# Optimization experiments

Hardware: AMD Instinct MI355X
Metric: run time of the kernel (lower is better)

The kernel has to match this reference:

```python
import jax, jax.numpy as jnp
import numpy as np

HIDDEN = 2048
NUM_HEADS = 16
KEY_DIM = 1024      # hidden * expand_k (0.5)
VALUE_DIM = 2048    # hidden * expand_v (1.0)
HEAD_K = KEY_DIM // NUM_HEADS   # 64
HEAD_V = VALUE_DIM // NUM_HEADS # 128
EPS = 1e-5
B, T = 8, 4096


def _rmsnorm(x, w, eps=EPS):
    var = jnp.mean(jnp.square(x), axis=-1, keepdims=True)
    return x * jax.lax.rsqrt(var + eps) * w


def setup_inputs() -> dict:
    key = jax.random.key(0)
    ks = jax.random.split(key, 7)
    s = 1.0 / np.sqrt(HIDDEN)
    return {
        "hidden_states": jax.random.normal(ks[0], (B, T, HIDDEN), dtype=jnp.float32),
        "recurrent_state": jax.random.normal(ks[1], (B, NUM_HEADS, HEAD_K, HEAD_V), dtype=jnp.float32),
        "norm_w": jnp.ones((HIDDEN,), dtype=jnp.float32),
        "q_w": jax.random.uniform(ks[2], (KEY_DIM, HIDDEN), jnp.float32, -s, s),
        "v_norm_w": jnp.ones((HEAD_V,), dtype=jnp.float32),
        "o_w": jax.random.uniform(ks[3], (HIDDEN, VALUE_DIM), jnp.float32, -s, s),
        "gate_w": jax.random.uniform(ks[4], (HIDDEN, HIDDEN), jnp.float32, -s, s),
    }


def reference(hidden_states, recurrent_state, norm_w, q_w, v_norm_w, o_w, gate_w):
    x = _rmsnorm(hidden_states, norm_w)                       # (B,T,D)
    q = x @ q_w.T                                             # (B,T,KEY_DIM)
    q = q.reshape(*q.shape[:2], NUM_HEADS, HEAD_K)            # (B,T,H,K)
    # L2 normalize along last dim (F.normalize default eps=1e-12 on the norm)
    norm = jnp.maximum(jnp.linalg.norm(q, axis=-1, keepdims=True), 1e-12)
    q = q / norm
    o = jnp.einsum('bthk,bhkv->bthv', q, recurrent_state)     # (B,T,H,V)
    o = _rmsnorm(o, v_norm_w)
    o = o.reshape(*o.shape[:2], VALUE_DIM)                    # (B,T,VALUE_DIM)
    o = o @ o_w.T                                             # (B,T,D)
    gate = jax.nn.sigmoid(x @ gate_w.T)                       # (B,T,D)
    return gate * o
```

## Files before the change

kernel.cpp:

```cpp
#include <hip/hip_runtime.h>

typedef unsigned short u16;
typedef unsigned int u32;
typedef __attribute__((ext_vector_type(4))) float f32x4;
typedef __attribute__((ext_vector_type(8))) short short8;
typedef __attribute__((ext_vector_type(4))) short short4v;

#define HIDDEN 2048
#define NHEADS 16
#define KEYDIM 1024
#define VALDIM 2048
#define HEADK 64
#define HEADV 128
#define NBATCH 8
#define SEQ 4096
#define NTOK (NBATCH * SEQ)

__device__ __forceinline__ u16 f2bf(float f) {
  union { float f; u32 u; } c; c.f = f;
  u32 r = c.u + 0x7FFFu + ((c.u >> 16) & 1u);
  return (u16)(r >> 16);
}
__device__ __forceinline__ float bf2f(u16 h) {
  union { u32 u; float f; } c; c.u = ((u32)h) << 16;
  return c.f;
}

__global__ __launch_bounds__(256) void cast_bf16_k(const float* __restrict__ in,
                                                   u16* __restrict__ out, int n4) {
  int i = blockIdx.x * blockDim.x + threadIdx.x;
  if (i >= n4) return;
  f32x4 v = *(const f32x4*)(in + (size_t)i * 4);
  short4v o;
  o[0] = (short)f2bf(v[0]); o[1] = (short)f2bf(v[1]);
  o[2] = (short)f2bf(v[2]); o[3] = (short)f2bf(v[3]);
  *(short4v*)(out + (size_t)i * 4) = o;
}

__global__ __launch_bounds__(256) void rmsnorm_cast_k(const float* __restrict__ x,
                                                      const float* __restrict__ w,
                                                      u16* __restrict__ xb) {
  int r = blockIdx.x;
  int tid = threadIdx.x;
  const float* xp = x + (size_t)r * HIDDEN + tid * 8;
  f32x4 v0 = *(const f32x4*)xp;
  f32x4 v1 = *(const f32x4*)(xp + 4);
  float ss = v0[0]*v0[0]+v0[1]*v0[1]+v0[2]*v0[2]+v0[3]*v0[3]
           + v1[0]*v1[0]+v1[1]*v1[1]+v1[2]*v1[2]+v1[3]*v1[3];
  #pragma unroll
  for (int m = 32; m >= 1; m >>= 1) ss += __shfl_xor(ss, m);
  __shared__ float red[4];
  if ((tid & 63) == 0) red[tid >> 6] = ss;
  __syncthreads();
  float tot = red[0] + red[1] + red[2] + red[3];
  float inv = rsqrtf(tot * (1.0f / HIDDEN) + 1e-5f);
  const float* wp = w + tid * 8;
  f32x4 w0 = *(const f32x4*)wp;
  f32x4 w1 = *(const f32x4*)(wp + 4);
  short8 o;
  o[0] = (short)f2bf(v0[0] * inv * w0[0]);
  o[1] = (short)f2bf(v0[1] * inv * w0[1]);
  o[2] = (short)f2bf(v0[2] * inv * w0[2]);
  o[3] = (short)f2bf(v0[3] * inv * w0[3]);
  o[4] = (short)f2bf(v1[0] * inv * w1[0]);
  o[5] = (short)f2bf(v1[1] * inv * w1[1]);
  o[6] = (short)f2bf(v1[2] * inv * w1[2]);
  o[7] = (short)f2bf(v1[3] * inv * w1[3]);
  *(short8*)(xb + (size_t)r * HIDDEN + tid * 8) = o;
}


__device__ __forceinline__ void gload16(const u16* g, u16* l) {
  __builtin_amdgcn_global_load_lds((const __attribute__((address_space(1))) void*)g,
                                   (__attribute__((address_space(3))) void*)l, 16, 0, 0);
}

#define BAR()                                  \
  do {                                         \
    asm volatile("" ::: "memory");             \
    __builtin_amdgcn_s_barrier();              \
    asm volatile("" ::: "memory");             \
  } while (0)

template <int MODE>
__global__ __launch_bounds__(512, 2) void gemm1b_k(const u16* __restrict__ A,
                                                   const u16* __restrict__ Bw,
                                                   void* __restrict__ Cptr,
                                                   const u16* __restrict__ Gate,
                                                   int M, int N, int K) {
  extern __shared__ u16 lds[];
  const int tid = threadIdx.x;
  const int wid = tid >> 6;
  const int wm = wid >> 2;
  const int wn = wid & 3;
  const int l = tid & 63;
  const int lr = l & 15;
  const int kq = l >> 4;

  const int ntn = N >> 8;
  const int per = gridDim.x >> 3;
  const int b = blockIdx.x;
  const int sidx = (b & 7) * per + (b >> 3);
  const int mt = sidx / ntn;
  const int nt = sidx - mt * ntn;

  const u16* Ag = A + (size_t)(mt * 256) * K;
  const u16* Bg = Bw + (size_t)(nt * 256) * K;

  const int srow = tid >> 3;
  const int schunk = (tid & 7) ^ (srow & 7);

#define STAGE_A(c, h)                                                          \
  do {                                                                         \
    const u16* _s = Ag + (size_t)((h) * 128 + srow) * K + ((c) << 6) + schunk * 8; \
    u16* _d = lds + (((c) & 1) << 15) + (h) * 8192 + tid * 8;                  \
    gload16(_s, _d);                                                           \
    gload16(_s + (size_t)64 * K, _d + 4096);                                   \
  } while (0)
#define STAGE_B(c, h)                                                          \
  do {                                                                         \
    const u16* _s = Bg + (size_t)((h) * 128 + srow) * K + ((c) << 6) + schunk * 8; \
    u16* _d = lds + (((c) & 1) << 15) + 16384 + (h) * 8192 + tid * 8;          \
    gload16(_s, _d);                                                           \
    gload16(_s + (size_t)64 * K, _d + 4096);                                   \
  } while (0)

  const int c0s = (kq ^ (lr & 7)) << 3;
  const int c1s = ((4 + kq) ^ (lr & 7)) << 3;
  const int aRowBase = (wm * 128 + lr) * 64;
  const int bRowBase = (wn * 64 + lr) * 64;

  short8 afr[4][2];
  short8 bfr[2][2][2];
  f32x4 acc[8][4] = {};

  auto LDA = [&](int buf, int mh) {
    #pragma unroll
    for (int mi = 0; mi < 4; ++mi) {
      const u16* p = lds + (buf << 15) + aRowBase + (mh * 64 + mi * 16) * 64;
      afr[mi][0] = *(const short8*)(p + c0s);
      afr[mi][1] = *(const short8*)(p + c1s);
    }
  };
  auto LDB_ALL = [&](int buf) {
    #pragma unroll
    for (int nh = 0; nh < 2; ++nh) {
      #pragma unroll
      for (int ni = 0; ni < 2; ++ni) {
        const u16* p = lds + (buf << 15) + 16384 + bRowBase + ((nh * 2 + ni) * 16) * 64;
        bfr[nh][ni][0] = *(const short8*)(p + c0s);
        bfr[nh][ni][1] = *(const short8*)(p + c1s);
      }
    }
  };
  auto MMA = [&](int mh, int nh) {
    __builtin_amdgcn_s_setprio(1);
    #pragma unroll
    for (int mi = 0; mi < 4; ++mi) {
      #pragma unroll
      for (int ni = 0; ni < 2; ++ni) {
        int m = mh * 4 + mi, n = nh * 2 + ni;
        acc[m][n] = __builtin_amdgcn_mfma_f32_16x16x32_bf16(afr[mi][0], bfr[nh][ni][0], acc[m][n], 0, 0, 0);
        acc[m][n] = __builtin_amdgcn_mfma_f32_16x16x32_bf16(afr[mi][1], bfr[nh][ni][1], acc[m][n], 0, 0, 0);
      }
    }
    __builtin_amdgcn_s_setprio(0);
  };

  STAGE_A(0, 0); STAGE_A(0, 1);
  STAGE_B(0, 0); STAGE_B(0, 1);
  STAGE_B(1, 0); STAGE_B(1, 1);
  asm volatile("s_waitcnt vmcnt(4)" ::: "memory");
  BAR();

  const int NITER = K >> 7;
  for (int i = 0; i < NITER; ++i) {
    const int g = (i + 1 < NITER);
    const int cA = 2 * i + 1, c2 = 2 * i + 2, c3 = 2 * i + 3;

    LDB_ALL(0); LDA(0, 0);
    STAGE_A(cA, 0);
    BAR(); MMA(0, 0);
    STAGE_A(cA, 1);
    BAR(); MMA(0, 1);
    LDA(0, 1);
    if (g) STAGE_B(c2, 0);
    BAR(); MMA(1, 1);
    if (g) {
      STAGE_B(c2, 1);
      asm volatile("s_waitcnt vmcnt(4)" ::: "memory");
    } else {
      asm volatile("s_waitcnt vmcnt(0)" ::: "memory");
    }
    BAR(); MMA(1, 0);

    LDB_ALL(1); LDA(1, 0);
    if (g) STAGE_A(c2, 0);
    BAR(); MMA(0, 0);
    if (g) STAGE_A(c2, 1);
    BAR(); MMA(0, 1);
    LDA(1, 1);
    if (g) STAGE_B(c3, 0);
    BAR(); MMA(1, 1);
    if (g) {
      STAGE_B(c3, 1);
      asm volatile("s_waitcnt vmcnt(4)" ::: "memory");
    }
    BAR(); MMA(1, 0);
  }
#undef STAGE_A
#undef STAGE_B

  const int rowB = mt * 256 + wm * 128 + kq * 4;
  const int colB = nt * 256 + wn * 64 + lr;
  #pragma unroll
  for (int m = 0; m < 8; ++m) {
    #pragma unroll
    for (int n = 0; n < 4; ++n) {
      #pragma unroll
      for (int j = 0; j < 4; ++j) {
        int row = rowB + m * 16 + j;
        int col = colB + n * 16;
        size_t idx = (size_t)row * N + col;
        float v = acc[m][n][j];
        if constexpr (MODE == 0) {
          ((u16*)Cptr)[idx] = f2bf(v);
        } else if constexpr (MODE == 1) {
          ((u16*)Cptr)[idx] = f2bf(1.0f / (1.0f + __expf(-v)));
        } else if constexpr (MODE == 2) {
          ((float*)Cptr)[idx] = v * bf2f(Gate[idx]);
        } else if constexpr (MODE == 3) {
          ((float*)Cptr)[idx] = 1.0f / (1.0f + __expf(-v));
        } else {
          float* O = (float*)Cptr;
          O[idx] = O[idx] * v;
        }
      }
    }
  }
}

__global__ __launch_bounds__(256) void glaread_k(const u16* __restrict__ q,
                                                 const float* __restrict__ S,
                                                 const float* __restrict__ vw,
                                                 u16* __restrict__ omid) {
  int bh = blockIdx.x;
  int b = bh >> 4, h = bh & 15;
  int tid = threadIdx.x;
  int w = tid >> 6, l = tid & 63;
  int lr = l & 15, kq = l >> 4;

  const float* Sp = S + (size_t)bh * HEADK * HEADV;
  short8 bfrag[8][2];
  #pragma unroll
  for (int n = 0; n < 8; ++n) {
    #pragma unroll
    for (int s = 0; s < 2; ++s) {
      #pragma unroll
      for (int i = 0; i < 8; ++i)
        bfrag[n][s][i] =
            (short)f2bf(Sp[(size_t)(s * 32 + kq * 8 + i) * HEADV + n * 16 + lr]);
    }
  }
  float vwn[8];
  #pragma unroll
  for (int n = 0; n < 8; ++n) vwn[n] = vw[n * 16 + lr];

  #pragma unroll 1
  for (int it = 0; it < 8; ++it) {
    int t0 = blockIdx.y * 512 + it * 64 + w * 16;
    const u16* qp = q + (size_t)(b * SEQ + t0 + lr) * KEYDIM + h * HEADK;
    short8 a0 = *(const short8*)(qp + kq * 8);
    short8 a1 = *(const short8*)(qp + 32 + kq * 8);

    float ss = 0.f;
    #pragma unroll
    for (int i = 0; i < 8; ++i) {
      float x0 = bf2f((u16)a0[i]), x1 = bf2f((u16)a1[i]);
      ss += x0 * x0 + x1 * x1;
    }
    ss += __shfl_xor(ss, 16);
    ss += __shfl_xor(ss, 32);
    float sc = 1.0f / fmaxf(sqrtf(ss), 1e-12f);

    short8 an0, an1;
    #pragma unroll
    for (int i = 0; i < 8; ++i) {
      an0[i] = (short)f2bf(bf2f((u16)a0[i]) * sc);
      an1[i] = (short)f2bf(bf2f((u16)a1[i]) * sc);
    }

    f32x4 acc[8] = {};
    #pragma unroll
    for (int n = 0; n < 8; ++n) {
      acc[n] = __builtin_amdgcn_mfma_f32_16x16x32_bf16(an0, bfrag[n][0], acc[n], 0, 0, 0);
      acc[n] = __builtin_amdgcn_mfma_f32_16x16x32_bf16(an1, bfrag[n][1], acc[n], 0, 0, 0);
    }

    float part[4] = {0.f, 0.f, 0.f, 0.f};
    #pragma unroll
    for (int n = 0; n < 8; ++n) {
      #pragma unroll
      for (int j = 0; j < 4; ++j) part[j] += acc[n][j] * acc[n][j];
    }
    #pragma unroll
    for (int msk = 1; msk <= 8; msk <<= 1) {
      #pragma unroll
      for (int j = 0; j < 4; ++j) part[j] += __shfl_xor(part[j], msk);
    }
    #pragma unroll
    for (int j = 0; j < 4; ++j) {
      float inv = rsqrtf(part[j] * (1.0f / HEADV) + 1e-5f);
      int tok = t0 + kq * 4 + j;
      u16* op = omid + (size_t)(b * SEQ + tok) * VALDIM + h * HEADV;
      #pragma unroll
      for (int n = 0; n < 8; ++n)
        op[n * 16 + lr] = f2bf(acc[n][j] * inv * vwn[n]);
    }
  }
}

extern "C" void kernel_launch(void* const* d_in, const int* in_sizes, int n_in,
                              void* d_out, int out_size, void* d_ws, size_t ws_size,
                              hipStream_t stream) {
  const float* hs = (const float*)d_in[0];
  const float* S  = (const float*)d_in[1];
  const float* nw = (const float*)d_in[2];
  const float* qw = (const float*)d_in[3];
  const float* vw = (const float*)d_in[4];
  const float* ow = (const float*)d_in[5];
  const float* gw = (const float*)d_in[6];
  float* out = (float*)d_out;

  u16* xb   = (u16*)d_ws;
  u16* q    = xb + (size_t)NTOK * HIDDEN;
  u16* qwb  = q + (size_t)NTOK * KEYDIM;
  u16* owb  = qwb + (size_t)KEYDIM * HIDDEN;
  u16* gwb  = owb + (size_t)HIDDEN * VALDIM;
  u16* gatebuf = gwb + (size_t)HIDDEN * HIDDEN;
  u16* omid = xb;

  const size_t need = ((size_t)NTOK * HIDDEN * 2) * 2 + (size_t)NTOK * KEYDIM * 2 +
                      ((size_t)KEYDIM * HIDDEN + 2 * (size_t)HIDDEN * HIDDEN) * 2;
  const bool bigws = ws_size >= need;

  const size_t LDSB = 131072;

  cast_bf16_k<<<(KEYDIM * HIDDEN / 4 + 255) / 256, 256, 0, stream>>>(qw, qwb, KEYDIM * HIDDEN / 4);
  cast_bf16_k<<<(HIDDEN * VALDIM / 4 + 255) / 256, 256, 0, stream>>>(ow, owb, HIDDEN * VALDIM / 4);
  cast_bf16_k<<<(HIDDEN * HIDDEN / 4 + 255) / 256, 256, 0, stream>>>(gw, gwb, HIDDEN * HIDDEN / 4);

  rmsnorm_cast_k<<<NTOK, 256, 0, stream>>>(hs, nw, xb);

  gemm1b_k<0><<<dim3((NTOK / 256) * (KEYDIM / 256)), 512, LDSB, stream>>>(xb, qwb, q, nullptr, NTOK, KEYDIM, HIDDEN);

  if (bigws) {
    gemm1b_k<1><<<dim3((NTOK / 256) * (HIDDEN / 256)), 512, LDSB, stream>>>(xb, gwb, gatebuf, nullptr, NTOK, HIDDEN, HIDDEN);
  } else {
    gemm1b_k<3><<<dim3((NTOK / 256) * (HIDDEN / 256)), 512, LDSB, stream>>>(xb, gwb, out, nullptr, NTOK, HIDDEN, HIDDEN);
  }

  glaread_k<<<dim3(NBATCH * NHEADS, SEQ / 512), 256, 0, stream>>>(q, S, vw, omid);

  if (bigws) {
    gemm1b_k<2><<<dim3((NTOK / 256) * (HIDDEN / 256)), 512, LDSB, stream>>>(omid, owb, out, gatebuf, NTOK, HIDDEN, VALDIM);
  } else {
    gemm1b_k<4><<<dim3((NTOK / 256) * (HIDDEN / 256)), 512, LDSB, stream>>>(omid, owb, out, nullptr, NTOK, HIDDEN, VALDIM);
  }
}
```

Measured before the change: 809.8 us.

## Fuse q and gate projections into one GEMM with head-major q output

Places the bf16 q and gate weight matrices next to each other in the workspace so one GEMM with N=3072 computes both projections from the shared normalized input. The epilogue branches on tile column: q tiles are written in a per-(batch,head) transposed layout, gate tiles get a sigmoid. The read kernel then loads q contiguously per head. This removes one kernel launch and the repeated reads of the activation matrix, and improves locality in the read kernel, at the cost of scattered 2-byte epilogue stores for the q layout.

```diff
diff --git a/kernel.cpp b/kernel.cpp
--- a/kernel.cpp
+++ b/kernel.cpp
@@ -86,7 +86,7 @@
 __global__ __launch_bounds__(512, 2) void gemm1b_k(const u16* __restrict__ A,
                                                    const u16* __restrict__ Bw,
                                                    void* __restrict__ Cptr,
-                                                   const u16* __restrict__ Gate,
+                                                   u16* __restrict__ Aux,
                                                    int M, int N, int K) {
   extern __shared__ u16 lds[];
   const int tid = threadIdx.x;
@@ -221,26 +221,35 @@
       for (int j = 0; j < 4; ++j) {
         int row = rowB + m * 16 + j;
         int col = colB + n * 16;
-        size_t idx = (size_t)row * N + col;
         float v = acc[m][n][j];
-        if constexpr (MODE == 0) {
-          ((u16*)Cptr)[idx] = f2bf(v);
-        } else if constexpr (MODE == 1) {
-          ((u16*)Cptr)[idx] = f2bf(1.0f / (1.0f + __expf(-v)));
-        } else if constexpr (MODE == 2) {
-          ((float*)Cptr)[idx] = v * bf2f(Gate[idx]);
-        } else if constexpr (MODE == 3) {
-          ((float*)Cptr)[idx] = 1.0f / (1.0f + __expf(-v));
-        } else {
+        if constexpr (MODE == 2) {
+          size_t idx = (size_t)row * N + col;
+          ((float*)Cptr)[idx] = v * bf2f(Aux[idx]);
+        } else if constexpr (MODE == 4) {
+          size_t idx = (size_t)row * N + col;
           float* O = (float*)Cptr;
           O[idx] = O[idx] * v;
+        } else {
+          if (nt < 4) {
+            int h = col >> 6, k = col & 63;
+            int bb = row >> 12, tok = row & (SEQ - 1);
+            Aux[((size_t)(bb * NHEADS + h) * SEQ + tok) * HEADK + k] = f2bf(v);
+          } else {
+            int colg = col - 1024;
+            float sg = 1.0f / (1.0f + __expf(-v));
+            if constexpr (MODE == 5) {
+              ((u16*)Cptr)[(size_t)row * HIDDEN + colg] = f2bf(sg);
+            } else {
+              ((float*)Cptr)[(size_t)row * HIDDEN + colg] = sg;
+            }
+          }
         }
       }
     }
   }
 }
 
-__global__ __launch_bounds__(256) void glaread_k(const u16* __restrict__ q,
+__global__ __launch_bounds__(256) void glaread_k(const u16* __restrict__ qT,
                                                  const float* __restrict__ S,
                                                  const float* __restrict__ vw,
                                                  u16* __restrict__ omid) {
@@ -266,10 +275,12 @@
   #pragma unroll
   for (int n = 0; n < 8; ++n) vwn[n] = vw[n * 16 + lr];
 
+  const u16* qbase = qT + (size_t)bh * SEQ * HEADK;
+
   #pragma unroll 1
   for (int it = 0; it < 8; ++it) {
     int t0 = blockIdx.y * 512 + it * 64 + w * 16;
-    const u16* qp = q + (size_t)(b * SEQ + t0 + lr) * KEYDIM + h * HEADK;
+    const u16* qp = qbase + (size_t)(t0 + lr) * HEADK;
     short8 a0 = *(const short8*)(qp + kq * 8);
     short8 a1 = *(const short8*)(qp + 32 + kq * 8);
 
@@ -333,11 +344,11 @@
   float* out = (float*)d_out;
 
   u16* xb   = (u16*)d_ws;
-  u16* q    = xb + (size_t)NTOK * HIDDEN;
-  u16* qwb  = q + (size_t)NTOK * KEYDIM;
-  u16* owb  = qwb + (size_t)KEYDIM * HIDDEN;
-  u16* gwb  = owb + (size_t)HIDDEN * VALDIM;
-  u16* gatebuf = gwb + (size_t)HIDDEN * HIDDEN;
+  u16* qT   = xb + (size_t)NTOK * HIDDEN;
+  u16* qwb  = qT + (size_t)NTOK * KEYDIM;
+  u16* gwb  = qwb + (size_t)KEYDIM * HIDDEN;
+  u16* owb  = gwb + (size_t)HIDDEN * HIDDEN;
+  u16* gatebuf = owb + (size_t)HIDDEN * VALDIM;
   u16* omid = xb;
 
   const size_t need = ((size_t)NTOK * HIDDEN * 2) * 2 + (size_t)NTOK * KEYDIM * 2 +
@@ -347,24 +358,26 @@
   const size_t LDSB = 131072;
 
   cast_bf16_k<<<(KEYDIM * HIDDEN / 4 + 255) / 256, 256, 0, stream>>>(qw, qwb, KEYDIM * HIDDEN / 4);
+  cast_bf16_k<<<(HIDDEN * HIDDEN / 4 + 255) / 256, 256, 0, stream>>>(gw, gwb, HIDDEN * HIDDEN / 4);
   cast_bf16_k<<<(HIDDEN * VALDIM / 4 + 255) / 256, 256, 0, stream>>>(ow, owb, HIDDEN * VALDIM / 4);
-  cast_bf16_k<<<(HIDDEN * HIDDEN / 4 + 255) / 256, 256, 0, stream>>>(gw, gwb, HIDDEN * HIDDEN / 4);
 
   rmsnorm_cast_k<<<NTOK, 256, 0, stream>>>(hs, nw, xb);
 
-  gemm1b_k<0><<<dim3((NTOK / 256) * (KEYDIM / 256)), 512, LDSB, stream>>>(xb, qwb, q, nullptr, NTOK, KEYDIM, HIDDEN);
-
   if (bigws) {
-    gemm1b_k<1><<<dim3((NTOK / 256) * (HIDDEN / 256)), 512, LDSB, stream>>>(xb, gwb, gatebuf, nullptr, NTOK, HIDDEN, HIDDEN);
+    gemm1b_k<5><<<dim3((NTOK / 256) * ((KEYDIM + HIDDEN) / 256)), 512, LDSB, stream>>>(
+        xb, qwb, gatebuf, qT, NTOK, KEYDIM + HIDDEN, HIDDEN);
   } else {
-    gemm1b_k<3><<<dim3((NTOK / 256) * (HIDDEN / 256)), 512, LDSB, stream>>>(xb, gwb, out, nullptr, NTOK, HIDDEN, HIDDEN);
-  }
-
-  glaread_k<<<dim3(NBATCH * NHEADS, SEQ / 512), 256, 0, stream>>>(q, S, vw, omid);
+    gemm1b_k<6><<<dim3((NTOK / 256) * ((KEYDIM + HIDDEN) / 256)), 512, LDSB, stream>>>(
+        xb, qwb, out, qT, NTOK, KEYDIM + HIDDEN, HIDDEN);
+  }
+
+  glaread_k<<<dim3(NBATCH * NHEADS, SEQ / 512), 256, 0, stream>>>(qT, S, vw, omid);
 
   if (bigws) {
-    gemm1b_k<2><<<dim3((NTOK / 256) * (HIDDEN / 256)), 512, LDSB, stream>>>(omid, owb, out, gatebuf, NTOK, HIDDEN, VALDIM);
+    gemm1b_k<2><<<dim3((NTOK / 256) * (HIDDEN / 256)), 512, LDSB, stream>>>(
+        omid, owb, out, gatebuf, NTOK, HIDDEN, VALDIM);
   } else {
-    gemm1b_k<4><<<dim3((NTOK / 256) * (HIDDEN / 256)), 512, LDSB, stream>>>(omid, owb, out, nullptr, NTOK, HIDDEN, VALDIM);
-  }
-}
+    gemm1b_k<4><<<dim3((NTOK / 256) * (HIDDEN / 256)), 512, LDSB, stream>>>(
+        omid, owb, out, nullptr, NTOK, HIDDEN, VALDIM);
+  }
+}
```

New measurement: 819.6 us. No clear change (+1.2%).
